# Optimization experiments

Measured on AMD Instinct MI355X. Metric: run time of the kernel, lower is better.

The kernel has to match this reference:

```python
import jax, jax.numpy as jnp
import numpy as np

N_NODES = 100000
N_EDGES = 3200000
D_FEAT = 128
UNITS = 128
EPS = 0.0


def setup_inputs() -> dict:
    key = jax.random.key(0)
    k1, k2, k3, k4, k5 = jax.random.split(key, 5)
    X = jax.random.normal(k1, (N_NODES, D_FEAT), dtype=jnp.float32)
    ref_A = jax.random.randint(k2, (N_EDGES,), 0, N_NODES, dtype=jnp.int32)  # dst per edge
    ref_B = jax.random.randint(k3, (N_EDGES,), 0, N_NODES, dtype=jnp.int32)  # src per edge
    # Glorot-uniform weights, zero biases (as in build())
    lim1 = float(np.sqrt(6.0 / (D_FEAT + UNITS)))
    lim2 = float(np.sqrt(6.0 / (UNITS + UNITS)))
    w1 = jax.random.uniform(k4, (D_FEAT, UNITS), minval=-lim1, maxval=lim1, dtype=jnp.float32)
    b1 = jnp.zeros((UNITS,), dtype=jnp.float32)
    w2 = jax.random.uniform(k5, (UNITS, UNITS), minval=-lim2, maxval=lim2, dtype=jnp.float32)
    b2 = jnp.zeros((UNITS,), dtype=jnp.float32)
    return {"X": X, "ref_A": ref_A, "ref_B": ref_B, "w1": w1, "b1": b1, "w2": w2, "b2": b2}


def reference(X, ref_A, ref_B, w1, b1, w2, b2):
    # c.convolution: gather source-node features and scatter-add to destinations
    agg = jax.ops.segment_sum(X[ref_B], ref_A, num_segments=N_NODES)  # [N, d]
    conv_X = (1.0 + EPS) * X + agg
    h = jax.nn.relu(conv_X @ w1 + b1)  # [N, units]
    out = jax.nn.relu(h @ w2 + b2)     # [N, units]
    return out
```

## Files before the change

kernel.cpp:

```cpp
#include <hip/hip_runtime.h>
#include <hip/hip_bf16.h>

#define NNODES 100000
#define DFEAT 128
#define NBKT 8
#define STRIPE 12500
#define BUCKET_CAP 416000
#define CHUNK 4096
#define SUBNODES 64
#define NSUB 196
#define SUBCAP 2560
#define NSB (NBKT * NSUB)

typedef short bf16x8 __attribute__((ext_vector_type(8)));
typedef float f32x4  __attribute__((ext_vector_type(4)));

__device__ __forceinline__ unsigned short f2bf(float f) {
    unsigned u = __builtin_bit_cast(unsigned, f);
    return (unsigned short)((u + 0x7fffu + ((u >> 16) & 1u)) >> 16);
}

__global__ __launch_bounds__(256)
void x2bf_kernel(const float4* __restrict__ X, uint4* __restrict__ Xb, int n8) {
    int i = blockIdx.x * 256 + threadIdx.x;
    if (i >= n8) return;
    float4 a = X[2 * i], b = X[2 * i + 1];
    uint4 o;
    o.x = f2bf(a.x) | ((unsigned)f2bf(a.y) << 16);
    o.y = f2bf(a.z) | ((unsigned)f2bf(a.w) << 16);
    o.z = f2bf(b.x) | ((unsigned)f2bf(b.y) << 16);
    o.w = f2bf(b.z) | ((unsigned)f2bf(b.w) << 16);
    Xb[i] = o;
}

__global__ __launch_bounds__(256)
void wprep(const float* __restrict__ w1, const float* __restrict__ w2,
           unsigned short* __restrict__ w1t, unsigned short* __restrict__ w2t) {
    int i = blockIdx.x * 256 + threadIdx.x;
    const float* w = (i < 16384) ? w1 : w2;
    unsigned short* o = (i < 16384) ? w1t : w2t;
    int j = i & 16383;
    int n = j >> 7, k = j & 127;
    o[n * 128 + k] = f2bf(w[k * 128 + n]);
}

__global__ __launch_bounds__(256)
void partition_edges(const int* __restrict__ dst, const int* __restrict__ src,
                     int* __restrict__ bcur, unsigned* __restrict__ bedges,
                     int nE) {
    __shared__ unsigned sbuf[CHUNK];
    __shared__ int scnt[NBKT];
    __shared__ int sbase[NBKT];
    __shared__ int scur[NBKT];
    __shared__ int gbase[NBKT];

    const int tid = threadIdx.x;
    const long long e0 = (long long)blockIdx.x * CHUNK;
    const int n = (int)min((long long)CHUNK, (long long)nE - e0);
    if (n <= 0) return;

    if (tid < NBKT) scnt[tid] = 0;
    __syncthreads();

    unsigned ent[CHUNK / 256];
    int bkt[CHUNK / 256];
#pragma unroll
    for (int j = 0; j < CHUNK / 256; ++j) {
        int i = tid + j * 256;
        if (i < n) {
            int d = dst[e0 + i];
            int s = src[e0 + i];
            int b = d / STRIPE;
            ent[j] = (unsigned)s | ((unsigned)(d - b * STRIPE) << 17);
            bkt[j] = b;
            atomicAdd(&scnt[b], 1);
        } else bkt[j] = -1;
    }
    __syncthreads();

    if (tid == 0) {
        int run = 0;
        for (int b = 0; b < NBKT; ++b) { sbase[b] = run; scur[b] = run; run += scnt[b]; }
    }
    __syncthreads();

#pragma unroll
    for (int j = 0; j < CHUNK / 256; ++j)
        if (bkt[j] >= 0) {
            int p = atomicAdd(&scur[bkt[j]], 1);
            sbuf[p] = ent[j];
        }
    if (tid < NBKT) gbase[tid] = atomicAdd(&bcur[tid], scnt[tid]);
    __syncthreads();

    for (int i = tid; i < n; i += 256) {
        int b = 0;
        while (b < NBKT - 1 && i >= sbase[b + 1]) ++b;
        bedges[(size_t)b * BUCKET_CAP + gbase[b] + (i - sbase[b])] = sbuf[i];
    }
}

__global__ __launch_bounds__(256)
void partition_sub(const unsigned* __restrict__ bedges, const int* __restrict__ bcur,
                   int* __restrict__ scur2, unsigned* __restrict__ sub_edges) {
    __shared__ unsigned sbuf[CHUNK];
    __shared__ int scnt[NSUB];
    __shared__ int sbase[NSUB + 1];
    __shared__ int scur[NSUB];
    __shared__ int gbase[NSUB];

    const int b   = blockIdx.x & (NBKT - 1);
    const int blk = blockIdx.x >> 3;
    const int sz  = bcur[b];
    const int e0  = blk * CHUNK;
    if (e0 >= sz) return;
    const int n = min(CHUNK, sz - e0);
    const unsigned* p = bedges + (size_t)b * BUCKET_CAP + e0;
    const int tid = threadIdx.x;

    for (int i = tid; i < NSUB; i += 256) scnt[i] = 0;
    __syncthreads();

    unsigned ent[CHUNK / 256];
    int sbk[CHUNK / 256];
#pragma unroll
    for (int j = 0; j < CHUNK / 256; ++j) {
        int i = tid + j * 256;
        if (i < n) {
            unsigned v = p[i];
            int s = (int)(v >> 23);
            ent[j] = v;
            sbk[j] = s;
            atomicAdd(&scnt[s], 1);
        } else sbk[j] = -1;
    }
    __syncthreads();

    if (tid == 0) {
        int run = 0;
        for (int s = 0; s < NSUB; ++s) { sbase[s] = run; scur[s] = run; run += scnt[s]; }
        sbase[NSUB] = run;
    }
    __syncthreads();

#pragma unroll
    for (int j = 0; j < CHUNK / 256; ++j)
        if (sbk[j] >= 0) {
            int pos = atomicAdd(&scur[sbk[j]], 1);
            sbuf[pos] = ent[j];
        }
    if (tid < NSUB) gbase[tid] = atomicAdd(&scur2[b * NSUB + tid], scnt[tid]);
    __syncthreads();

    for (int s = 0; s < NSUB; ++s) {
        int lo = sbase[s], hi = sbase[s + 1];
        int g0 = gbase[s];
        unsigned* q = sub_edges + (size_t)(b * NSUB + s) * SUBCAP;
        for (int i = lo + tid; i < hi; i += 256) {
            int o = g0 + (i - lo);
            if (o < SUBCAP) q[o] = sbuf[i];
        }
    }
}

__device__ __forceinline__ void bfadd(float* acc, uint4 v) {
    acc[0] += __builtin_bit_cast(float, v.x << 16);
    acc[1] += __builtin_bit_cast(float, v.x & 0xffff0000u);
    acc[2] += __builtin_bit_cast(float, v.y << 16);
    acc[3] += __builtin_bit_cast(float, v.y & 0xffff0000u);
    acc[4] += __builtin_bit_cast(float, v.z << 16);
    acc[5] += __builtin_bit_cast(float, v.z & 0xffff0000u);
    acc[6] += __builtin_bit_cast(float, v.w << 16);
    acc[7] += __builtin_bit_cast(float, v.w & 0xffff0000u);
}

__global__ __launch_bounds__(256, 8)
void sort_aggregate(const unsigned* __restrict__ sub_edges,
                    const int* __restrict__ scur2,
                    const uint4* __restrict__ Xb, uint4* __restrict__ convb) {
    __shared__ unsigned srt[SUBCAP];
    __shared__ int cnt[SUBNODES];
    __shared__ int off[SUBNODES + 1];
    __shared__ int cur[SUBNODES];

    const int b  = blockIdx.x & (NBKT - 1);
    const int j  = blockIdx.x >> 3;
    const int sb = b * NSUB + j;
    const int tid = threadIdx.x;
    const int sz = min(scur2[sb], SUBCAP);
    const int nodeBase = b * STRIPE + j * SUBNODES;
    const int nLoc = min(SUBNODES, STRIPE - j * SUBNODES);
    const unsigned* p = sub_edges + (size_t)sb * SUBCAP;

    if (tid < SUBNODES) cnt[tid] = 0;
    __syncthreads();
    for (int i = tid; i < sz; i += 256)
        atomicAdd(&cnt[(p[i] >> 17) & 63], 1);
    __syncthreads();

    if (tid < 64) {
        int v = cnt[tid];
        int s = v;
#pragma unroll
        for (int d = 1; d < 64; d <<= 1) {
            int t = __shfl_up(s, d, 64);
            if (tid >= d) s += t;
        }
        off[tid + 1] = s;
        cur[tid] = s - v;
        if (tid == 0) off[0] = 0;
    }
    __syncthreads();

    for (int i = tid; i < sz; i += 256) {
        unsigned v = p[i];
        int pos = atomicAdd(&cur[(v >> 17) & 63], 1);
        srt[pos] = v & 0x1FFFFu;
    }
    __syncthreads();

    const int grp = tid >> 4, lane = tid & 15;
    for (int n0 = grp; n0 < nLoc; n0 += 16) {
        int node = nodeBase + n0;
        float acc[8];
#pragma unroll
        for (int q = 0; q < 8; ++q) acc[q] = 0.f;
        bfadd(acc, Xb[(size_t)node * 16 + lane]);

        int e = off[n0], end = off[n0 + 1];
        for (; e + 4 <= end; e += 4) {
            int s0 = srt[e + 0], s1 = srt[e + 1], s2 = srt[e + 2], s3 = srt[e + 3];
            uint4 v0 = Xb[(size_t)s0 * 16 + lane];
            uint4 v1 = Xb[(size_t)s1 * 16 + lane];
            uint4 v2 = Xb[(size_t)s2 * 16 + lane];
            uint4 v3 = Xb[(size_t)s3 * 16 + lane];
            bfadd(acc, v0); bfadd(acc, v1); bfadd(acc, v2); bfadd(acc, v3);
        }
        for (; e < end; ++e)
            bfadd(acc, Xb[(size_t)srt[e] * 16 + lane]);

        uint4 o;
        o.x = f2bf(acc[0]) | ((unsigned)f2bf(acc[1]) << 16);
        o.y = f2bf(acc[2]) | ((unsigned)f2bf(acc[3]) << 16);
        o.z = f2bf(acc[4]) | ((unsigned)f2bf(acc[5]) << 16);
        o.w = f2bf(acc[6]) | ((unsigned)f2bf(acc[7]) << 16);
        convb[(size_t)node * 16 + lane] = o;
    }
}

#define TM 128

__global__ __launch_bounds__(256, 1)
void mlp_fused(const unsigned short* __restrict__ convb,
               const unsigned short* __restrict__ w1t, const float* __restrict__ b1,
               const unsigned short* __restrict__ w2t, const float* __restrict__ b2,
               float* __restrict__ out, int N) {
    __shared__ unsigned short sA[TM][136];
    __shared__ unsigned short sW[128][136];
    __shared__ unsigned short sH[TM][136];

    const int tid  = threadIdx.x;
    const int row0 = blockIdx.x * TM;

    for (int i = tid; i < TM * 16; i += 256) {
        int r = i >> 4, c = i & 15;
        uint4 v = make_uint4(0, 0, 0, 0);
        if (row0 + r < N) v = ((const uint4*)convb)[(size_t)(row0 + r) * 16 + c];
        *(uint4*)&sA[r][c * 8] = v;
    }
    for (int i = tid; i < 128 * 16; i += 256) {
        int r = i >> 4, c = i & 15;
        *(uint4*)&sW[r][c * 8] = ((const uint4*)w1t)[r * 16 + c];
    }
    __syncthreads();

    const int lane = tid & 63;
    const int lrow = lane & 15;
    const int kgrp = lane >> 4;
    const int m0   = (tid >> 6) * 32;

    float bias[8];
#pragma unroll
    for (int nf = 0; nf < 8; ++nf) bias[nf] = b1[nf * 16 + lrow];

    f32x4 acc[2][8] = {};
#pragma unroll
    for (int kk = 0; kk < 128; kk += 32) {
        bf16x8 a0 = *(const bf16x8*)&sA[m0 + lrow][kk + kgrp * 8];
        bf16x8 a1 = *(const bf16x8*)&sA[m0 + 16 + lrow][kk + kgrp * 8];
#pragma unroll
        for (int nf = 0; nf < 8; ++nf) {
            bf16x8 b = *(const bf16x8*)&sW[nf * 16 + lrow][kk + kgrp * 8];
            acc[0][nf] = __builtin_amdgcn_mfma_f32_16x16x32_bf16(a0, b, acc[0][nf], 0, 0, 0);
            acc[1][nf] = __builtin_amdgcn_mfma_f32_16x16x32_bf16(a1, b, acc[1][nf], 0, 0, 0);
        }
    }

#pragma unroll
    for (int mf = 0; mf < 2; ++mf)
#pragma unroll
        for (int nf = 0; nf < 8; ++nf)
#pragma unroll
            for (int r = 0; r < 4; ++r) {
                int row = m0 + mf * 16 + kgrp * 4 + r;
                int col = nf * 16 + lrow;
                float h = fmaxf(acc[mf][nf][r] + bias[nf], 0.f);
                sH[row][col] = f2bf(h);
            }

    __syncthreads();

    for (int i = tid; i < 128 * 16; i += 256) {
        int r = i >> 4, c = i & 15;
        *(uint4*)&sW[r][c * 8] = ((const uint4*)w2t)[r * 16 + c];
    }
#pragma unroll
    for (int nf = 0; nf < 8; ++nf) bias[nf] = b2[nf * 16 + lrow];
#pragma unroll
    for (int mf = 0; mf < 2; ++mf)
#pragma unroll
        for (int nf = 0; nf < 8; ++nf) acc[mf][nf] = (f32x4){0.f, 0.f, 0.f, 0.f};
    __syncthreads();

#pragma unroll
    for (int kk = 0; kk < 128; kk += 32) {
        bf16x8 a0 = *(const bf16x8*)&sH[m0 + lrow][kk + kgrp * 8];
        bf16x8 a1 = *(const bf16x8*)&sH[m0 + 16 + lrow][kk + kgrp * 8];
#pragma unroll
        for (int nf = 0; nf < 8; ++nf) {
            bf16x8 b = *(const bf16x8*)&sW[nf * 16 + lrow][kk + kgrp * 8];
            acc[0][nf] = __builtin_amdgcn_mfma_f32_16x16x32_bf16(a0, b, acc[0][nf], 0, 0, 0);
            acc[1][nf] = __builtin_amdgcn_mfma_f32_16x16x32_bf16(a1, b, acc[1][nf], 0, 0, 0);
        }
    }

#pragma unroll
    for (int mf = 0; mf < 2; ++mf)
#pragma unroll
        for (int nf = 0; nf < 8; ++nf)
#pragma unroll
            for (int r = 0; r < 4; ++r) {
                int row = row0 + m0 + mf * 16 + kgrp * 4 + r;
                int col = nf * 16 + lrow;
                if (row < N)
                    out[(size_t)row * 128 + col] = fmaxf(acc[mf][nf][r] + bias[nf], 0.f);
            }
}

extern "C" void kernel_launch(void* const* d_in, const int* in_sizes, int n_in,
                              void* d_out, int out_size, void* d_ws, size_t ws_size,
                              hipStream_t stream) {
    const float* X    = (const float*)d_in[0];
    const int*   refA = (const int*)d_in[1];
    const int*   refB = (const int*)d_in[2];
    const float* w1   = (const float*)d_in[3];
    const float* b1   = (const float*)d_in[4];
    const float* w2   = (const float*)d_in[5];
    const float* b2   = (const float*)d_in[6];
    float* out = (float*)d_out;

    const int nNodes = in_sizes[0] / DFEAT;
    const int nE     = in_sizes[1];

    char* ws = (char*)d_ws;
    unsigned short* Xb    = (unsigned short*)ws;  ws += (size_t)nNodes * DFEAT * 2;
    unsigned short* convb = (unsigned short*)ws;
    unsigned* bedges      = (unsigned*)convb;
    ws += (size_t)nNodes * DFEAT * 2;
    unsigned* sub_edges = (unsigned*)ws;          ws += (size_t)NSB * SUBCAP * 4;
    unsigned short* w1t = (unsigned short*)ws;    ws += 16384 * 2;
    unsigned short* w2t = (unsigned short*)ws;    ws += 16384 * 2;
    int* bcur  = (int*)ws;                        ws += 64 * 4;
    int* scur2 = (int*)ws;

    int n8 = nNodes * DFEAT / 8;
    x2bf_kernel<<<(n8 + 255) / 256, 256, 0, stream>>>((const float4*)X, (uint4*)Xb, n8);
    wprep<<<128, 256, 0, stream>>>(w1, w2, w1t, w2t);

    hipMemsetAsync(bcur, 0, (64 + NSB) * 4, stream);
    int pBlocks = (nE + CHUNK - 1) / CHUNK;
    partition_edges<<<pBlocks, 256, 0, stream>>>(refA, refB, bcur, bedges, nE);
    partition_sub<<<(BUCKET_CAP / CHUNK + 1) * NBKT, 256, 0, stream>>>(
        bedges, bcur, scur2, sub_edges);

    sort_aggregate<<<NSB, 256, 0, stream>>>(sub_edges, scur2,
                                            (const uint4*)Xb, (uint4*)convb);

    int mBlocks = (nNodes + TM - 1) / TM;
    mlp_fused<<<mBlocks, 256, 0, stream>>>(convb, w1t, b1, w2t, b2, out, nNodes);
}
```

Measured before the change: 252.2 us.

## Merge prep kernels and memset, wave-split sub-bucket writes, reuse smem in MLP

Folds the bf16 conversion of X, the weight transpose and the counter zeroing into one launch, removing two launches and a memset. In partition_sub, each wave now writes a different sub-bucket and empty sub-buckets are skipped, where before all 256 threads walked every sub-bucket in turn. The MLP kernel writes the hidden activations back into sA instead of a separate sH buffer, cutting shared memory so two blocks can fit per CU (launch bounds raised to 2). The extra occupancy may cost registers or cause spills.

```diff
diff --git a/kernel.cpp b/kernel.cpp
--- a/kernel.cpp
+++ b/kernel.cpp
@@ -21,27 +21,32 @@
 }
 
 __global__ __launch_bounds__(256)
-void x2bf_kernel(const float4* __restrict__ X, uint4* __restrict__ Xb, int n8) {
-    int i = blockIdx.x * 256 + threadIdx.x;
-    if (i >= n8) return;
-    float4 a = X[2 * i], b = X[2 * i + 1];
-    uint4 o;
-    o.x = f2bf(a.x) | ((unsigned)f2bf(a.y) << 16);
-    o.y = f2bf(a.z) | ((unsigned)f2bf(a.w) << 16);
-    o.z = f2bf(b.x) | ((unsigned)f2bf(b.y) << 16);
-    o.w = f2bf(b.z) | ((unsigned)f2bf(b.w) << 16);
-    Xb[i] = o;
-}
-
-__global__ __launch_bounds__(256)
-void wprep(const float* __restrict__ w1, const float* __restrict__ w2,
-           unsigned short* __restrict__ w1t, unsigned short* __restrict__ w2t) {
-    int i = blockIdx.x * 256 + threadIdx.x;
-    const float* w = (i < 16384) ? w1 : w2;
-    unsigned short* o = (i < 16384) ? w1t : w2t;
-    int j = i & 16383;
-    int n = j >> 7, k = j & 127;
-    o[n * 128 + k] = f2bf(w[k * 128 + n]);
+void prep_all(const float4* __restrict__ X, uint4* __restrict__ Xb, int n8, int n8b,
+              const float* __restrict__ w1, const float* __restrict__ w2,
+              unsigned short* __restrict__ w1t, unsigned short* __restrict__ w2t,
+              int* __restrict__ zbase) {
+    const int bid = blockIdx.x;
+    const int tid = threadIdx.x;
+    if (bid < n8b) {
+        int i = bid * 256 + tid;
+        if (i >= n8) return;
+        float4 a = X[2 * i], b = X[2 * i + 1];
+        uint4 o;
+        o.x = f2bf(a.x) | ((unsigned)f2bf(a.y) << 16);
+        o.y = f2bf(a.z) | ((unsigned)f2bf(a.w) << 16);
+        o.z = f2bf(b.x) | ((unsigned)f2bf(b.y) << 16);
+        o.w = f2bf(b.z) | ((unsigned)f2bf(b.w) << 16);
+        Xb[i] = o;
+    } else if (bid < n8b + 128) {
+        int i = (bid - n8b) * 256 + tid;
+        const float* w = (i < 16384) ? w1 : w2;
+        unsigned short* o = (i < 16384) ? w1t : w2t;
+        int j = i & 16383;
+        int n = j >> 7, k = j & 127;
+        o[n * 128 + k] = f2bf(w[k * 128 + n]);
+    } else {
+        for (int i = tid; i < 64 + NSB; i += 256) zbase[i] = 0;
+    }
 }
 
 __global__ __launch_bounds__(256)
@@ -152,11 +157,13 @@
     if (tid < NSUB) gbase[tid] = atomicAdd(&scur2[b * NSUB + tid], scnt[tid]);
     __syncthreads();
 
-    for (int s = 0; s < NSUB; ++s) {
+    const int wave = tid >> 6, lane = tid & 63;
+    for (int s = wave; s < NSUB; s += 4) {
         int lo = sbase[s], hi = sbase[s + 1];
+        if (lo == hi) continue;
         int g0 = gbase[s];
         unsigned* q = sub_edges + (size_t)(b * NSUB + s) * SUBCAP;
-        for (int i = lo + tid; i < hi; i += 256) {
+        for (int i = lo + lane; i < hi; i += 64) {
             int o = g0 + (i - lo);
             if (o < SUBCAP) q[o] = sbuf[i];
         }
@@ -250,14 +257,13 @@
 
 #define TM 128
 
-__global__ __launch_bounds__(256, 1)
+__global__ __launch_bounds__(256, 2)
 void mlp_fused(const unsigned short* __restrict__ convb,
                const unsigned short* __restrict__ w1t, const float* __restrict__ b1,
                const unsigned short* __restrict__ w2t, const float* __restrict__ b2,
                float* __restrict__ out, int N) {
     __shared__ unsigned short sA[TM][136];
     __shared__ unsigned short sW[128][136];
-    __shared__ unsigned short sH[TM][136];
 
     const int tid  = threadIdx.x;
     const int row0 = blockIdx.x * TM;
@@ -305,7 +311,7 @@
                 int row = m0 + mf * 16 + kgrp * 4 + r;
                 int col = nf * 16 + lrow;
                 float h = fmaxf(acc[mf][nf][r] + bias[nf], 0.f);
-                sH[row][col] = f2bf(h);
+                sA[row][col] = f2bf(h);
             }
 
     __syncthreads();
@@ -324,8 +330,8 @@
 
 #pragma unroll
     for (int kk = 0; kk < 128; kk += 32) {
-        bf16x8 a0 = *(const bf16x8*)&sH[m0 + lrow][kk + kgrp * 8];
-        bf16x8 a1 = *(const bf16x8*)&sH[m0 + 16 + lrow][kk + kgrp * 8];
+        bf16x8 a0 = *(const bf16x8*)&sA[m0 + lrow][kk + kgrp * 8];
+        bf16x8 a1 = *(const bf16x8*)&sA[m0 + 16 + lrow][kk + kgrp * 8];
 #pragma unroll
         for (int nf = 0; nf < 8; ++nf) {
             bf16x8 b = *(const bf16x8*)&sW[nf * 16 + lrow][kk + kgrp * 8];
@@ -373,11 +379,11 @@
     int* bcur  = (int*)ws;                        ws += 64 * 4;
     int* scur2 = (int*)ws;
 
-    int n8 = nNodes * DFEAT / 8;
-    x2bf_kernel<<<(n8 + 255) / 256, 256, 0, stream>>>((const float4*)X, (uint4*)Xb, n8);
-    wprep<<<128, 256, 0, stream>>>(w1, w2, w1t, w2t);
-
-    hipMemsetAsync(bcur, 0, (64 + NSB) * 4, stream);
+    int n8  = nNodes * DFEAT / 8;
+    int n8b = (n8 + 255) / 256;
+    prep_all<<<n8b + 128 + 1, 256, 0, stream>>>((const float4*)X, (uint4*)Xb, n8, n8b,
+                                                w1, w2, w1t, w2t, bcur);
+
     int pBlocks = (nE + CHUNK - 1) / CHUNK;
     partition_edges<<<pBlocks, 256, 0, stream>>>(refA, refB, bcur, bedges, nE);
     partition_sub<<<(BUCKET_CAP / CHUNK + 1) * NBKT, 256, 0, stream>>>(
```

Result: faster. 211.3 us (-16.2%).
